# Kernel optimization log

Measured on AMD Instinct MI355X. Metric: run time of the kernel, lower is better.

Reference implementation:

```python
import jax, jax.numpy as jnp
import numpy as np

N_DRUG, N_DIS, E, D = 10000, 15000, 1048576, 128

def setup_inputs() -> dict:
    key = jax.random.key(0)
    k = jax.random.split(key, 6)
    return {
        "z_drug": jax.random.normal(k[0], (N_DRUG, D), dtype=jnp.float32),
        "z_disease": jax.random.normal(k[1], (N_DIS, D), dtype=jnp.float32),
        "row": jax.random.randint(k[2], (E,), 0, N_DRUG),
        "col": jax.random.randint(k[3], (E,), 0, N_DIS),
        "W1": jax.random.normal(k[4], (2 * D, D), dtype=jnp.float32) * (1.0 / np.sqrt(2 * D)),
        "b1": jnp.zeros((D,), dtype=jnp.float32),
        "W2": jax.random.normal(k[5], (D, 1), dtype=jnp.float32) * (1.0 / np.sqrt(D)),
        "b2": jnp.zeros((1,), dtype=jnp.float32),
    }

def reference(z_drug, z_disease, row, col, W1, b1, W2, b2):
    # gather per-edge embeddings and concatenate: [E, 2D]
    z = jnp.concatenate([z_drug[row], z_disease[col]], axis=-1)
    h = jax.nn.relu(z @ W1 + b1)          # [E, D]
    out = h @ W2 + b2                      # [E, 1]
    return out.reshape(-1)                 # [E]
```

## Files before the change

### kernel.cpp

```cpp
#include <hip/hip_runtime.h>

typedef __attribute__((ext_vector_type(8))) short short8;
typedef __attribute__((ext_vector_type(4))) float floatx4;
typedef _Float16 half8 __attribute__((ext_vector_type(8)));
typedef _Float16 half4 __attribute__((ext_vector_type(4)));
typedef _Float16 half2v __attribute__((ext_vector_type(2)));

static __device__ __forceinline__ unsigned short f2bf(float x) {
    unsigned int u = __builtin_bit_cast(unsigned int, x);
    unsigned int r = (u + 0x7FFFu + ((u >> 16) & 1u)) >> 16;
    return (unsigned short)r;
}

static __device__ void phase_gemm(
    int b, const float* __restrict__ zd, const float* __restrict__ zs,
    const float* __restrict__ W1, const float* __restrict__ b1,
    _Float16* __restrict__ ud, _Float16* __restrict__ us,
    int ndrows, int nsrows, int ntd)
{
    const int tid  = threadIdx.x;
    const int lane = tid & 63;
    const int wave = tid >> 6;
    const int wh   = wave >> 1;
    const int we   = wave & 1;
    const int l15  = lane & 15;
    const int quad = lane >> 4;

    const bool isD = (b < ntd);
    const float* __restrict__ z = isD ? zd : zs;
    _Float16* __restrict__ u = isD ? ud : us;
    const int nrows = isD ? ndrows : nsrows;
    const int m0    = (isD ? b : b - ntd) * 64;
    const int koff0 = isD ? 0 : 128;
    const int whbase = wh * 64;

    short8 wfrag[16];
    #pragma unroll
    for (int s = 0; s < 4; ++s)
        #pragma unroll
        for (int mt = 0; mt < 4; ++mt) {
            short8 t;
            #pragma unroll
            for (int j = 0; j < 8; ++j)
                t[j] = (short)f2bf(
                    W1[(size_t)(koff0 + s * 32 + quad * 8 + j) * 128 +
                       whbase + mt * 16 + l15]);
            wfrag[s * 4 + mt] = t;
        }

    floatx4 acc[2][4];
    #pragma unroll
    for (int mt = 0; mt < 4; ++mt) {
        floatx4 bb = *reinterpret_cast<const floatx4*>(&b1[whbase + mt * 16 + quad * 4]);
        bb *= 0.5f;
        acc[0][mt] = bb;
        acc[1][mt] = bb;
    }

    int rowi[2], rowc[2];
    #pragma unroll
    for (int et = 0; et < 2; ++et) {
        rowi[et] = m0 + we * 32 + et * 16 + l15;
        rowc[et] = rowi[et] < nrows ? rowi[et] : nrows - 1;
    }

    #pragma unroll
    for (int s = 0; s < 4; ++s) {
        short8 bf[2];
        #pragma unroll
        for (int et = 0; et < 2; ++et) {
            const float* src = &z[(size_t)rowc[et] * 128 + s * 32 + quad * 8];
            floatx4 lo = *reinterpret_cast<const floatx4*>(src);
            floatx4 hi = *reinterpret_cast<const floatx4*>(src + 4);
            short8 t;
            t[0] = (short)f2bf(lo[0]); t[1] = (short)f2bf(lo[1]);
            t[2] = (short)f2bf(lo[2]); t[3] = (short)f2bf(lo[3]);
            t[4] = (short)f2bf(hi[0]); t[5] = (short)f2bf(hi[1]);
            t[6] = (short)f2bf(hi[2]); t[7] = (short)f2bf(hi[3]);
            bf[et] = t;
        }
        #pragma unroll
        for (int et = 0; et < 2; ++et)
            #pragma unroll
            for (int mt = 0; mt < 4; ++mt)
                acc[et][mt] = __builtin_amdgcn_mfma_f32_16x16x32_bf16(
                    wfrag[s * 4 + mt], bf[et], acc[et][mt], 0, 0, 0);
    }

    #pragma unroll
    for (int et = 0; et < 2; ++et) {
        if (rowi[et] < nrows) {
            #pragma unroll
            for (int mt = 0; mt < 4; ++mt) {
                half4 hv;
                #pragma unroll
                for (int rr = 0; rr < 4; ++rr) hv[rr] = (_Float16)acc[et][mt][rr];
                *reinterpret_cast<half4*>(
                    &u[(size_t)rowi[et] * 128 + whbase + mt * 16 + quad * 4]) = hv;
            }
        }
    }
}

static __device__ void phase_hist(
    int hb, const int* __restrict__ row, const int* __restrict__ col,
    unsigned* __restrict__ ghist, int E, int nbrow, int colh)
{
    __shared__ unsigned lh[1280];
    const int tid = threadIdx.x;
    for (int i = tid; i < 1280; i += 256) lh[i] = 0;
    __syncthreads();
    const int per = (E + 191) / 192;
    const int e0 = hb * per;
    int e1 = e0 + per; if (e1 > E) e1 = E;
    for (int e = e0 + tid; e < e1; e += 256) {
        int r = row[e], c = col[e];
        int bin = ((c >= colh) ? nbrow : 0) + (r >> 4);
        atomicAdd(&lh[bin], 1u);
    }
    __syncthreads();
    const int nb = 2 * nbrow;
    for (int i = tid; i < nb; i += 256) {
        unsigned v = lh[i];
        if (v) atomicAdd(&ghist[i], v);
    }
}

__global__ __launch_bounds__(256, 2) void k_mid(
    const float* __restrict__ zd, const float* __restrict__ zs,
    const float* __restrict__ W1, const float* __restrict__ b1,
    _Float16* __restrict__ ud, _Float16* __restrict__ us,
    int ndrows, int nsrows, int ntd, int nbg,
    const int* __restrict__ row, const int* __restrict__ col,
    unsigned* __restrict__ ghist, int E, int nbrow, int colh)
{
    const int b = blockIdx.x;
    if (b < nbg) phase_gemm(b, zd, zs, W1, b1, ud, us, ndrows, nsrows, ntd);
    else         phase_hist(b - nbg, row, col, ghist, E, nbrow, colh);
}

__global__ void k_scan(const unsigned* __restrict__ ghist, unsigned* __restrict__ gcur,
                       unsigned* __restrict__ gmeta, int nb, int nbrow)
{
    __shared__ unsigned tsum[256];
    const int tid = threadIdx.x;
    unsigned v[5];
    unsigned s = 0;
    #pragma unroll
    for (int i = 0; i < 5; ++i) {
        int idx = tid * 5 + i;
        v[i] = (idx < nb) ? ghist[idx] : 0u;
        s += v[i];
    }
    tsum[tid] = s;
    for (int off = 1; off < 256; off <<= 1) {
        __syncthreads();
        unsigned y = (tid >= off) ? tsum[tid - off] : 0u;
        __syncthreads();
        tsum[tid] += y;
    }
    __syncthreads();
    unsigned running = tsum[tid] - s;
    #pragma unroll
    for (int i = 0; i < 5; ++i) {
        int idx = tid * 5 + i;
        if (idx < nb) {
            gcur[idx] = running;
            if (idx == nbrow) gmeta[0] = running;
            running += v[i];
        }
    }
}

__global__ __launch_bounds__(256, 4) void k_scatter(
    const int* __restrict__ row, const int* __restrict__ col,
    unsigned* __restrict__ gcur, unsigned long long* __restrict__ recbuf,
    int E, int nbrow, int colh)
{
    __shared__ unsigned lh[1280];
    const int tid = threadIdx.x;
    for (int i = tid; i < 1280; i += 256) lh[i] = 0;
    __syncthreads();

    const int per = E >> 9;
    const long base = (long)blockIdx.x * per;

    unsigned rnk[8], rcv[8];
    int binv[8];
    #pragma unroll
    for (int k = 0; k < 8; ++k) {
        long e = base + k * 256 + tid;
        int r = row[e], c = col[e];
        rcv[k] = (unsigned)r | ((unsigned)c << 14);
        binv[k] = ((c >= colh) ? nbrow : 0) + (r >> 4);
        rnk[k] = atomicAdd(&lh[binv[k]], 1u);
    }
    __syncthreads();
    const int nb = 2 * nbrow;
    for (int i = tid; i < nb; i += 256) {
        unsigned cnt = lh[i];
        if (cnt) lh[i] = atomicAdd(&gcur[i], cnt);
    }
    __syncthreads();
    #pragma unroll
    for (int k = 0; k < 8; ++k) {
        long e = base + k * 256 + tid;
        unsigned pos = lh[binv[k]] + rnk[k];
        recbuf[pos] = (unsigned long long)rcv[k] | ((unsigned long long)(unsigned)e << 32);
    }
}

__global__ __launch_bounds__(256, 4) void k_edge(
    const _Float16* __restrict__ ud, const _Float16* __restrict__ us,
    const unsigned* __restrict__ gmeta, const unsigned long long* __restrict__ recbuf,
    const float* __restrict__ w2, const float* __restrict__ b2,
    float* __restrict__ out, int E)
{
    const int tid  = threadIdx.x;
    const int lane = tid & 63;
    const int wave = tid >> 6;
    const int le   = lane >> 3;
    const int q    = lane & 7;
    const int lslot = wave * 8 + le;

    const int b   = blockIdx.x;
    const int cc  = (b & 7) >> 2;
    const int sub = ((b >> 3) << 2) | (b & 3);
    const unsigned n0 = gmeta[0];
    const unsigned c0 = cc ? n0 : 0u;
    const unsigned nc = cc ? ((unsigned)E - n0) : n0;
    if (nc == 0) return;
    const unsigned K = (nc + 511u) >> 9;
    unsigned start = c0 + (unsigned)sub * K;
    unsigned climit = c0 + nc;
    if (start >= climit) return;
    unsigned end = start + K;
    if (end > climit) end = climit;

#if __has_builtin(__builtin_amdgcn_fdot2)
    half2v w2h[8];
    #pragma unroll
    for (int i = 0; i < 2; ++i)
        #pragma unroll
        for (int p = 0; p < 4; ++p) {
            half2v t;
            t[0] = (_Float16)w2[i * 64 + q * 8 + 2 * p];
            t[1] = (_Float16)w2[i * 64 + q * 8 + 2 * p + 1];
            w2h[i * 4 + p] = t;
        }
#else
    float w2r[16];
    #pragma unroll
    for (int i = 0; i < 2; ++i) {
        *reinterpret_cast<floatx4*>(&w2r[i * 8]) =
            *reinterpret_cast<const floatx4*>(&w2[i * 64 + q * 8]);
        *reinterpret_cast<floatx4*>(&w2r[i * 8 + 4]) =
            *reinterpret_cast<const floatx4*>(&w2[i * 64 + q * 8 + 4]);
    }
#endif
    const float b2v = b2[0];
    const int tend = (int)((end - start + 31u) >> 5);

#define LOADREC(RV, VV, tt)                                                    \
    {                                                                          \
        unsigned ei = start + (unsigned)(tt) * 32u + (unsigned)lslot;          \
        VV = ei < end;                                                         \
        RV = recbuf[VV ? ei : start];                                          \
    }

#define GATHER(D, RV)                                                          \
    {                                                                          \
        unsigned r = (unsigned)(RV) & 16383u;                                  \
        unsigned c = ((unsigned)(RV) >> 14) & 16383u;                          \
        const _Float16* up = ud + (size_t)r * 128 + q * 8;                     \
        const _Float16* vp = us + (size_t)c * 128 + q * 8;                     \
        D[0] = *reinterpret_cast<const half8*>(up);                            \
        D[1] = *reinterpret_cast<const half8*>(up + 64);                       \
        D[2] = *reinterpret_cast<const half8*>(vp);                            \
        D[3] = *reinterpret_cast<const half8*>(vp + 64);                       \
    }

#if __has_builtin(__builtin_amdgcn_fdot2)
#define DOTBODY(D, accv)                                                       \
    half8 s0 = D[0] + D[2];                                                    \
    s0 = __builtin_elementwise_max(s0, (half8)(_Float16)0.f);                  \
    half8 s1 = D[1] + D[3];                                                    \
    s1 = __builtin_elementwise_max(s1, (half8)(_Float16)0.f);                  \
    _Pragma("unroll")                                                          \
    for (int p = 0; p < 4; ++p) {                                              \
        half2v pr0; pr0[0] = s0[2 * p]; pr0[1] = s0[2 * p + 1];                \
        accv = __builtin_amdgcn_fdot2(pr0, w2h[p], accv, false);               \
        half2v pr1; pr1[0] = s1[2 * p]; pr1[1] = s1[2 * p + 1];                \
        accv = __builtin_amdgcn_fdot2(pr1, w2h[4 + p], accv, false);           \
    }
#else
#define DOTBODY(D, accv)                                                       \
    half8 s0 = D[0] + D[2];                                                    \
    s0 = __builtin_elementwise_max(s0, (half8)(_Float16)0.f);                  \
    half8 s1 = D[1] + D[3];                                                    \
    s1 = __builtin_elementwise_max(s1, (half8)(_Float16)0.f);                  \
    _Pragma("unroll")                                                          \
    for (int j = 0; j < 8; ++j) {                                              \
        accv += (float)s0[j] * w2r[j];                                         \
        accv += (float)s1[j] * w2r[8 + j];                                     \
    }
#endif

#define COMPUTE(D, RV, VV)                                                     \
    {                                                                          \
        float acc = 0.f;                                                       \
        DOTBODY(D, acc)                                                        \
        acc += __shfl_xor(acc, 1);                                             \
        acc += __shfl_xor(acc, 2);                                             \
        acc += __shfl_xor(acc, 4);                                             \
        if ((VV) && q == 0) out[(unsigned)((RV) >> 32)] = acc + b2v;           \
    }

    unsigned long long recA, recB = 0, recA2 = 0, recB2 = 0;
    bool vA, vB = false, vA2 = false, vB2 = false;
    int t = 0;
    LOADREC(recA, vA, 0)
    bool hasB = (1 < tend);
    if (hasB) LOADREC(recB, vB, 1)

    half8 dA[4], dB[4];
    while (true) {
        GATHER(dA, recA)
        if (hasB) GATHER(dB, recB)

        bool hasA2 = (t + 2 < tend), hasB2 = (t + 3 < tend);
        if (hasA2) LOADREC(recA2, vA2, t + 2)
        if (hasB2) LOADREC(recB2, vB2, t + 3)

        COMPUTE(dA, recA, vA)
        if (!hasB) break;
        COMPUTE(dB, recB, vB)

        if (!hasA2) break;
        recA = recA2; vA = vA2;
        recB = recB2; vB = vB2;
        hasB = hasB2;
        t += 2;
    }
#undef LOADREC
#undef GATHER
#undef DOTBODY
#undef COMPUTE
}

extern "C" void kernel_launch(void* const* d_in, const int* in_sizes, int n_in,
                              void* d_out, int out_size, void* d_ws, size_t ws_size,
                              hipStream_t stream) {
    const float* zd = (const float*)d_in[0];
    const float* zs = (const float*)d_in[1];
    const int*   row = (const int*)d_in[2];
    const int*   col = (const int*)d_in[3];
    const float* W1 = (const float*)d_in[4];
    const float* b1 = (const float*)d_in[5];
    const float* w2 = (const float*)d_in[6];
    const float* b2 = (const float*)d_in[7];
    float* out = (float*)d_out;

    const int nd = in_sizes[0];
    const int ns = in_sizes[1];
    const int E  = in_sizes[2];
    const int ndrows = nd / 128;
    const int nsrows = ns / 128;
    const int nbrow = (ndrows + 15) >> 4;
    const int nb = 2 * nbrow;
    const int colh = nsrows >> 1;

    _Float16* ud = (_Float16*)d_ws;
    _Float16* us = ud + (size_t)ndrows * 128;
    size_t off = (size_t)((char*)(us + (size_t)nsrows * 128) - (char*)d_ws);
    off = (off + 63) & ~(size_t)63;
    unsigned* gmeta = (unsigned*)((char*)d_ws + off);
    unsigned* ghist = gmeta + 16;
    unsigned* gcur  = ghist + 1280;
    unsigned long long* recbuf =
        (unsigned long long*)(((uintptr_t)(gcur + 1280) + 63) & ~(uintptr_t)63);

    hipMemsetAsync(gmeta, 0, (16 + 1280) * sizeof(unsigned), stream);

    const int ntd = (ndrows + 63) / 64;
    const int nts = (nsrows + 63) / 64;
    const int nbg = ntd + nts;
    hipLaunchKernelGGL(k_mid, dim3(nbg + 192), dim3(256), 0, stream,
                       zd, zs, W1, b1, ud, us, ndrows, nsrows, ntd, nbg,
                       row, col, ghist, E, nbrow, colh);

    hipLaunchKernelGGL(k_scan, dim3(1), dim3(256), 0, stream,
                       ghist, gcur, gmeta, nb, nbrow);

    hipLaunchKernelGGL(k_scatter, dim3(512), dim3(256), 0, stream,
                       row, col, gcur, recbuf, E, nbrow, colh);

    hipLaunchKernelGGL(k_edge, dim3(1024), dim3(256), 0, stream,
                       ud, us, gmeta, recbuf, w2, b2, out, E);
}
```

Measured before the change: 152.3 us.

## Bucket edges by 64-drug-row bins and stage drug embeddings in LDS

Edges are now bucketed only by 64-row drug bins (157 bins), not 16-row bins split by disease half. The separate scan kernel is removed: each scatter block computes the prefix serially in thread 0, and each edge block reduces its own base offset. Each edge block loads its bin's 64 drug rows (16 KB fp16) into shared memory, so only the disease row is gathered from global memory per edge. The cost is a serial per-block prefix, higher LDS use per block with occupancy 8 requested, and possible load imbalance because blocks are assigned to bins by block index modulo bin count.

```diff
diff --git a/kernel.cpp b/kernel.cpp
--- a/kernel.cpp
+++ b/kernel.cpp
@@ -103,24 +103,21 @@
 }
 
 static __device__ void phase_hist(
-    int hb, const int* __restrict__ row, const int* __restrict__ col,
-    unsigned* __restrict__ ghist, int E, int nbrow, int colh)
-{
-    __shared__ unsigned lh[1280];
+    int hb, const int* __restrict__ row,
+    unsigned* __restrict__ ghist, int nbins)
+{
+    __shared__ unsigned lh[192];
     const int tid = threadIdx.x;
-    for (int i = tid; i < 1280; i += 256) lh[i] = 0;
-    __syncthreads();
-    const int per = (E + 191) / 192;
-    const int e0 = hb * per;
-    int e1 = e0 + per; if (e1 > E) e1 = E;
-    for (int e = e0 + tid; e < e1; e += 256) {
-        int r = row[e], c = col[e];
-        int bin = ((c >= colh) ? nbrow : 0) + (r >> 4);
-        atomicAdd(&lh[bin], 1u);
-    }
-    __syncthreads();
-    const int nb = 2 * nbrow;
-    for (int i = tid; i < nb; i += 256) {
+    for (int i = tid; i < nbins; i += 256) lh[i] = 0;
+    __syncthreads();
+    const long base = (long)hb * 2048;
+    #pragma unroll
+    for (int k = 0; k < 8; ++k) {
+        int r = row[base + k * 256 + tid];
+        atomicAdd(&lh[r >> 6], 1u);
+    }
+    __syncthreads();
+    for (int i = tid; i < nbins; i += 256) {
         unsigned v = lh[i];
         if (v) atomicAdd(&ghist[i], v);
     }
@@ -131,60 +128,27 @@
     const float* __restrict__ W1, const float* __restrict__ b1,
     _Float16* __restrict__ ud, _Float16* __restrict__ us,
     int ndrows, int nsrows, int ntd, int nbg,
-    const int* __restrict__ row, const int* __restrict__ col,
-    unsigned* __restrict__ ghist, int E, int nbrow, int colh)
+    const int* __restrict__ row,
+    unsigned* __restrict__ ghist, int nbins)
 {
     const int b = blockIdx.x;
     if (b < nbg) phase_gemm(b, zd, zs, W1, b1, ud, us, ndrows, nsrows, ntd);
-    else         phase_hist(b - nbg, row, col, ghist, E, nbrow, colh);
-}
-
-__global__ void k_scan(const unsigned* __restrict__ ghist, unsigned* __restrict__ gcur,
-                       unsigned* __restrict__ gmeta, int nb, int nbrow)
-{
-    __shared__ unsigned tsum[256];
-    const int tid = threadIdx.x;
-    unsigned v[5];
-    unsigned s = 0;
-    #pragma unroll
-    for (int i = 0; i < 5; ++i) {
-        int idx = tid * 5 + i;
-        v[i] = (idx < nb) ? ghist[idx] : 0u;
-        s += v[i];
-    }
-    tsum[tid] = s;
-    for (int off = 1; off < 256; off <<= 1) {
-        __syncthreads();
-        unsigned y = (tid >= off) ? tsum[tid - off] : 0u;
-        __syncthreads();
-        tsum[tid] += y;
-    }
-    __syncthreads();
-    unsigned running = tsum[tid] - s;
-    #pragma unroll
-    for (int i = 0; i < 5; ++i) {
-        int idx = tid * 5 + i;
-        if (idx < nb) {
-            gcur[idx] = running;
-            if (idx == nbrow) gmeta[0] = running;
-            running += v[i];
-        }
-    }
+    else         phase_hist(b - nbg, row, ghist, nbins);
 }
 
 __global__ __launch_bounds__(256, 4) void k_scatter(
     const int* __restrict__ row, const int* __restrict__ col,
-    unsigned* __restrict__ gcur, unsigned long long* __restrict__ recbuf,
-    int E, int nbrow, int colh)
-{
-    __shared__ unsigned lh[1280];
+    const unsigned* __restrict__ ghist, unsigned* __restrict__ gcur,
+    unsigned long long* __restrict__ recbuf, int nbins)
+{
+    __shared__ unsigned pb[192];
+    __shared__ unsigned lcnt[192];
+    __shared__ unsigned gt[192];
     const int tid = threadIdx.x;
-    for (int i = tid; i < 1280; i += 256) lh[i] = 0;
-    __syncthreads();
-
-    const int per = E >> 9;
-    const long base = (long)blockIdx.x * per;
-
+    for (int i = tid; i < nbins; i += 256) lcnt[i] = 0;
+    __syncthreads();
+
+    const long base = (long)blockIdx.x * 2048;
     unsigned rnk[8], rcv[8];
     int binv[8];
     #pragma unroll
@@ -192,30 +156,37 @@
         long e = base + k * 256 + tid;
         int r = row[e], c = col[e];
         rcv[k] = (unsigned)r | ((unsigned)c << 14);
-        binv[k] = ((c >= colh) ? nbrow : 0) + (r >> 4);
-        rnk[k] = atomicAdd(&lh[binv[k]], 1u);
-    }
-    __syncthreads();
-    const int nb = 2 * nbrow;
-    for (int i = tid; i < nb; i += 256) {
-        unsigned cnt = lh[i];
-        if (cnt) lh[i] = atomicAdd(&gcur[i], cnt);
+        binv[k] = r >> 6;
+        rnk[k] = atomicAdd(&lcnt[binv[k]], 1u);
+    }
+    __syncthreads();
+    if (tid == 0) {
+        unsigned run = 0;
+        for (int i = 0; i < nbins; ++i) { pb[i] = run; run += ghist[i]; }
+    }
+    for (int i = tid; i < nbins; i += 256) {
+        unsigned cnt = lcnt[i];
+        if (cnt) gt[i] = atomicAdd(&gcur[i], cnt);
     }
     __syncthreads();
     #pragma unroll
     for (int k = 0; k < 8; ++k) {
         long e = base + k * 256 + tid;
-        unsigned pos = lh[binv[k]] + rnk[k];
+        unsigned pos = pb[binv[k]] + gt[binv[k]] + rnk[k];
         recbuf[pos] = (unsigned long long)rcv[k] | ((unsigned long long)(unsigned)e << 32);
     }
 }
 
-__global__ __launch_bounds__(256, 4) void k_edge(
+__global__ __launch_bounds__(256, 8) void k_edge(
     const _Float16* __restrict__ ud, const _Float16* __restrict__ us,
-    const unsigned* __restrict__ gmeta, const unsigned long long* __restrict__ recbuf,
+    const unsigned* __restrict__ ghist, const unsigned long long* __restrict__ recbuf,
     const float* __restrict__ w2, const float* __restrict__ b2,
-    float* __restrict__ out, int E)
-{
+    float* __restrict__ out, int ndrows, int nbins)
+{
+    __shared__ _Float16 uL[64 * 128];
+    __shared__ unsigned red[256];
+    __shared__ unsigned sh_base, sh_cnt;
+
     const int tid  = threadIdx.x;
     const int lane = tid & 63;
     const int wave = tid >> 6;
@@ -223,19 +194,28 @@
     const int q    = lane & 7;
     const int lslot = wave * 8 + le;
 
+    const int G   = (int)gridDim.x;
     const int b   = blockIdx.x;
-    const int cc  = (b & 7) >> 2;
-    const int sub = ((b >> 3) << 2) | (b & 3);
-    const unsigned n0 = gmeta[0];
-    const unsigned c0 = cc ? n0 : 0u;
-    const unsigned nc = cc ? ((unsigned)E - n0) : n0;
-    if (nc == 0) return;
-    const unsigned K = (nc + 511u) >> 9;
-    unsigned start = c0 + (unsigned)sub * K;
-    unsigned climit = c0 + nc;
-    if (start >= climit) return;
-    unsigned end = start + K;
-    if (end > climit) end = climit;
+    const int bin = b % nbins;
+    const int w   = b / nbins;
+    const int nwq = G / nbins, nwr = G % nbins;
+    const int nwb = nwq + (bin < nwr ? 1 : 0);
+
+    red[tid] = (tid < bin) ? ghist[tid] : 0u;
+    __syncthreads();
+    for (int off = 128; off > 0; off >>= 1) {
+        if (tid < off) red[tid] += red[tid + off];
+        __syncthreads();
+    }
+    if (tid == 0) { sh_base = red[0]; sh_cnt = ghist[bin]; }
+
+    const int r0 = bin << 6;
+    int nr = ndrows - r0; if (nr > 64) nr = 64;
+    for (int i = tid; i < nr * 16; i += 256) {
+        int rr = i >> 4, pp = i & 15;
+        *reinterpret_cast<half8*>(&uL[rr * 128 + pp * 8]) =
+            *reinterpret_cast<const half8*>(&ud[(size_t)(r0 + rr) * 128 + pp * 8]);
+    }
 
 #if __has_builtin(__builtin_amdgcn_fdot2)
     half2v w2h[8];
@@ -259,57 +239,65 @@
     }
 #endif
     const float b2v = b2[0];
-    const int tend = (int)((end - start + 31u) >> 5);
+    __syncthreads();
+
+    const unsigned base = sh_base;
+    const unsigned cnt  = sh_cnt;
+    const unsigned K  = (cnt + (unsigned)nwb - 1u) / (unsigned)nwb;
+    unsigned s0 = (unsigned)w * K;
+    if (s0 >= cnt) return;
+    unsigned s1 = s0 + K; if (s1 > cnt) s1 = cnt;
+    const int tend = (int)((s1 - s0 + 31u) >> 5);
 
 #define LOADREC(RV, VV, tt)                                                    \
     {                                                                          \
-        unsigned ei = start + (unsigned)(tt) * 32u + (unsigned)lslot;          \
-        VV = ei < end;                                                         \
-        RV = recbuf[VV ? ei : start];                                          \
+        unsigned li = s0 + (unsigned)(tt) * 32u + (unsigned)lslot;             \
+        VV = li < s1;                                                          \
+        RV = recbuf[base + (VV ? li : s0)];                                    \
     }
 
 #define GATHER(D, RV)                                                          \
     {                                                                          \
-        unsigned r = (unsigned)(RV) & 16383u;                                  \
         unsigned c = ((unsigned)(RV) >> 14) & 16383u;                          \
-        const _Float16* up = ud + (size_t)r * 128 + q * 8;                     \
         const _Float16* vp = us + (size_t)c * 128 + q * 8;                     \
-        D[0] = *reinterpret_cast<const half8*>(up);                            \
-        D[1] = *reinterpret_cast<const half8*>(up + 64);                       \
-        D[2] = *reinterpret_cast<const half8*>(vp);                            \
-        D[3] = *reinterpret_cast<const half8*>(vp + 64);                       \
+        D[0] = *reinterpret_cast<const half8*>(vp);                            \
+        D[1] = *reinterpret_cast<const half8*>(vp + 64);                       \
     }
 
 #if __has_builtin(__builtin_amdgcn_fdot2)
-#define DOTBODY(D, accv)                                                       \
-    half8 s0 = D[0] + D[2];                                                    \
-    s0 = __builtin_elementwise_max(s0, (half8)(_Float16)0.f);                  \
-    half8 s1 = D[1] + D[3];                                                    \
-    s1 = __builtin_elementwise_max(s1, (half8)(_Float16)0.f);                  \
+#define DOTBODY(D, RV, accv)                                                   \
+    const unsigned rl = ((unsigned)(RV) & 16383u) - (unsigned)r0;              \
+    const _Float16* up = &uL[rl * 128 + q * 8];                                \
+    half8 s0v = *reinterpret_cast<const half8*>(up) + D[0];                    \
+    s0v = __builtin_elementwise_max(s0v, (half8)(_Float16)0.f);                \
+    half8 s1v = *reinterpret_cast<const half8*>(up + 64) + D[1];               \
+    s1v = __builtin_elementwise_max(s1v, (half8)(_Float16)0.f);                \
     _Pragma("unroll")                                                          \
     for (int p = 0; p < 4; ++p) {                                              \
-        half2v pr0; pr0[0] = s0[2 * p]; pr0[1] = s0[2 * p + 1];                \
+        half2v pr0; pr0[0] = s0v[2 * p]; pr0[1] = s0v[2 * p + 1];              \
         accv = __builtin_amdgcn_fdot2(pr0, w2h[p], accv, false);               \
-        half2v pr1; pr1[0] = s1[2 * p]; pr1[1] = s1[2 * p + 1];                \
+        half2v pr1; pr1[0] = s1v[2 * p]; pr1[1] = s1v[2 * p + 1];              \
         accv = __builtin_amdgcn_fdot2(pr1, w2h[4 + p], accv, false);           \
     }
 #else
-#define DOTBODY(D, accv)                                                       \
-    half8 s0 = D[0] + D[2];                                                    \
-    s0 = __builtin_elementwise_max(s0, (half8)(_Float16)0.f);                  \
-    half8 s1 = D[1] + D[3];                                                    \
-    s1 = __builtin_elementwise_max(s1, (half8)(_Float16)0.f);                  \
+#define DOTBODY(D, RV, accv)                                                   \
+    const unsigned rl = ((unsigned)(RV) & 16383u) - (unsigned)r0;              \
+    const _Float16* up = &uL[rl * 128 + q * 8];                                \
+    half8 s0v = *reinterpret_cast<const half8*>(up) + D[0];                    \
+    s0v = __builtin_elementwise_max(s0v, (half8)(_Float16)0.f);                \
+    half8 s1v = *reinterpret_cast<const half8*>(up + 64) + D[1];               \
+    s1v = __builtin_elementwise_max(s1v, (half8)(_Float16)0.f);                \
     _Pragma("unroll")                                                          \
     for (int j = 0; j < 8; ++j) {                                              \
-        accv += (float)s0[j] * w2r[j];                                         \
-        accv += (float)s1[j] * w2r[8 + j];                                     \
+        accv += (float)s0v[j] * w2r[j];                                        \
+        accv += (float)s1v[j] * w2r[8 + j];                                    \
     }
 #endif
 
 #define COMPUTE(D, RV, VV)                                                     \
     {                                                                          \
         float acc = 0.f;                                                       \
-        DOTBODY(D, acc)                                                        \
+        DOTBODY(D, RV, acc)                                                    \
         acc += __shfl_xor(acc, 1);                                             \
         acc += __shfl_xor(acc, 2);                                             \
         acc += __shfl_xor(acc, 4);                                             \
@@ -323,7 +311,7 @@
     bool hasB = (1 < tend);
     if (hasB) LOADREC(recB, vB, 1)
 
-    half8 dA[4], dB[4];
+    half8 dA[2], dB[2];
     while (true) {
         GATHER(dA, recA)
         if (hasB) GATHER(dB, recB)
@@ -366,35 +354,30 @@
     const int E  = in_sizes[2];
     const int ndrows = nd / 128;
     const int nsrows = ns / 128;
-    const int nbrow = (ndrows + 15) >> 4;
-    const int nb = 2 * nbrow;
-    const int colh = nsrows >> 1;
+
+    const int nbins = (ndrows + 63) >> 6;
 
     _Float16* ud = (_Float16*)d_ws;
     _Float16* us = ud + (size_t)ndrows * 128;
     size_t off = (size_t)((char*)(us + (size_t)nsrows * 128) - (char*)d_ws);
     off = (off + 63) & ~(size_t)63;
-    unsigned* gmeta = (unsigned*)((char*)d_ws + off);
-    unsigned* ghist = gmeta + 16;
-    unsigned* gcur  = ghist + 1280;
-    unsigned long long* recbuf =
-        (unsigned long long*)(((uintptr_t)(gcur + 1280) + 63) & ~(uintptr_t)63);
-
-    hipMemsetAsync(gmeta, 0, (16 + 1280) * sizeof(unsigned), stream);
+    unsigned* ghist = (unsigned*)((char*)d_ws + off);
+    unsigned* gcur  = ghist + 192;
+    unsigned long long* recbuf = (unsigned long long*)
+        (((uintptr_t)(gcur + 192) + 63) & ~(uintptr_t)63);
+
+    hipMemsetAsync(ghist, 0, 384 * sizeof(unsigned), stream);
 
     const int ntd = (ndrows + 63) / 64;
     const int nts = (nsrows + 63) / 64;
     const int nbg = ntd + nts;
-    hipLaunchKernelGGL(k_mid, dim3(nbg + 192), dim3(256), 0, stream,
+    hipLaunchKernelGGL(k_mid, dim3(nbg + E / 2048), dim3(256), 0, stream,
                        zd, zs, W1, b1, ud, us, ndrows, nsrows, ntd, nbg,
-                       row, col, ghist, E, nbrow, colh);
-
-    hipLaunchKernelGGL(k_scan, dim3(1), dim3(256), 0, stream,
-                       ghist, gcur, gmeta, nb, nbrow);
-
-    hipLaunchKernelGGL(k_scatter, dim3(512), dim3(256), 0, stream,
-                       row, col, gcur, recbuf, E, nbrow, colh);
-
-    hipLaunchKernelGGL(k_edge, dim3(1024), dim3(256), 0, stream,
-                       ud, us, gmeta, recbuf, w2, b2, out, E);
-}
+                       row, ghist, nbins);
+
+    hipLaunchKernelGGL(k_scatter, dim3(E / 2048), dim3(256), 0, stream,
+                       row, col, ghist, gcur, recbuf, nbins);
+
+    hipLaunchKernelGGL(k_edge, dim3(2048), dim3(256), 0, stream,
+                       ud, us, ghist, recbuf, w2, b2, out, ndrows, nbins);
+}
```

After: 148.1 us. 2.8% less time.
